# Kernel tuning notes

Measured on AMD Instinct MI355X. Metric: run time of the kernel, lower is better.

Reference implementation:

```python
import jax, jax.numpy as jnp
import numpy as np
from jax import lax

VOCAB, EMBED, HIDDEN, OUT = 256, 256, 512, 256
B, T = 256, 1024


def setup_inputs() -> dict:
    key = jax.random.key(0)
    k1, k2, k3, k4, k5, k6 = jax.random.split(key, 6)
    x = jax.random.randint(k1, (B, T), 0, VOCAB)
    h = jnp.zeros((B, HIDDEN), dtype=jnp.float32)
    emb = jax.random.normal(k2, (VOCAB, EMBED), dtype=jnp.float32)
    # torch Linear weights are [out_features, in_features]
    W = jax.random.normal(k3, (HIDDEN, EMBED + HIDDEN), dtype=jnp.float32) * 0.02
    b = jax.random.normal(k4, (HIDDEN,), dtype=jnp.float32) * 0.02
    Wd = jax.random.normal(k5, (OUT, HIDDEN), dtype=jnp.float32) * 0.02
    bd = jax.random.normal(k6, (OUT,), dtype=jnp.float32) * 0.02
    return {"x": x, "h": h, "emb": emb, "W": W, "b": b, "Wd": Wd, "bd": bd}


def reference(x, h, emb, W, b, Wd, bd):
    # Embed all timesteps at once: [B, T, E] -> time-major [T, B, E]
    ex = jnp.swapaxes(emb[x], 0, 1)

    # Split recurrent weight into input and hidden parts so concat is a sum of GEMMs.
    Wx = W[:, :EMBED]      # [H, E]
    Wh = W[:, EMBED:]      # [H, H]

    def step(h_prev, e_t):
        h_next = jnp.tanh(e_t @ Wx.T + h_prev @ Wh.T + b)
        return h_next, h_next

    h_final, hs = lax.scan(step, h, ex)          # hs: [T, B, H]
    outputs = jnp.swapaxes(hs, 0, 1) @ Wd.T + bd  # [B, T, OUT]
    return outputs, h_final
```

## Files before the change

kernel.cpp:

```cpp
#include <hip/hip_runtime.h>

typedef float f32x4 __attribute__((ext_vector_type(4)));
typedef int i32x4 __attribute__((ext_vector_type(4)));

#define B_ 256
#define T_ 1024
#define H_ 512
#define E_ 256
#define O_ 256
#define V_ 256

__device__ __align__(16) unsigned g_P2[V_ * 256];
__device__ __align__(16) signed char    g_Whq[H_ * H_];
__device__ float                        g_scale[H_];
__device__ __align__(16) signed char    g_Wdq[O_ * H_];
__device__ float                        g_sd[O_];

__device__ __forceinline__ unsigned short f2bf(float f) {
    union { float f; unsigned int u; } v; v.f = f;
    unsigned int r = v.u + 0x7fffu + ((v.u >> 16) & 1u);
    return (unsigned short)(r >> 16);
}
__device__ __forceinline__ float bf2f(unsigned short s) {
    union { unsigned int u; float f; } v; v.u = ((unsigned int)s) << 16;
    return v.f;
}
#define SW16(r_) (((r_) & 15) << 4)

__global__ void k_embWx(const float* __restrict__ emb, const float* __restrict__ W,
                        const float* __restrict__ bb) {
    __shared__ float e[E_];
    int v = blockIdx.x;
    e[threadIdx.x] = emb[(size_t)v * E_ + threadIdx.x];
    __syncthreads();
#pragma unroll
    for (int rep = 0; rep < 2; rep++) {
        int n = threadIdx.x + rep * 256;
        const float4* wr4 = (const float4*)(W + (size_t)n * (E_ + H_));
        float s = bb[n];
        for (int k = 0; k < E_ / 4; k++) {
            float4 wv = wr4[k];
            s += e[4*k] * wv.x + e[4*k+1] * wv.y + e[4*k+2] * wv.z + e[4*k+3] * wv.w;
        }
        int w = n >> 6, r6 = n & 63;
        int lo = r6 & 15, nt = r6 >> 4;
        int p = nt >> 1, half = nt & 1;
        ((unsigned short*)g_P2)[(v * 256 + w * 32 + lo * 2 + p) * 2 + half] = f2bf(s);
    }
}

__global__ void k_prep8(const float* __restrict__ W) {
    const int n = blockIdx.x;
    const int li = threadIdx.x;
    const float* src = W + (size_t)n * (E_ + H_) + E_;
    float v[8];
    float mx = 0.f;
#pragma unroll
    for (int m = 0; m < 8; m++) { v[m] = src[li * 8 + m]; mx = fmaxf(mx, fabsf(v[m])); }
#pragma unroll
    for (int off = 1; off < 64; off <<= 1)
        mx = fmaxf(mx, __shfl_xor(mx, off));
    const float s = fmaxf(mx, 1e-20f) / 127.f;
    if (li == 0) g_scale[n] = s;
    const float inv = 1.f / s;
    unsigned long long pk = 0;
#pragma unroll
    for (int m = 0; m < 8; m++) {
        int q = __float2int_rn(v[m] * inv);
        q = q > 127 ? 127 : (q < -127 ? -127 : q);
        pk |= ((unsigned long long)(unsigned char)(signed char)q) << (8 * m);
    }
    const int ktt = li >> 3;
    const int hig = (li >> 1) & 3;
    const int jh = li & 1;
    *(unsigned long long*)(g_Whq + (((size_t)(n >> 4) * 8 + ktt) * 1024)
                           + ((n & 15) + (hig << 4)) * 16 + jh * 8) = pk;
}

__global__ void k_prepWd8(const float* __restrict__ Wd) {
    const int n = blockIdx.x;
    const int li = threadIdx.x;
    const float* src = Wd + (size_t)n * H_;
    float v[8];
    float mx = 0.f;
#pragma unroll
    for (int m = 0; m < 8; m++) { v[m] = src[li * 8 + m]; mx = fmaxf(mx, fabsf(v[m])); }
#pragma unroll
    for (int off = 1; off < 64; off <<= 1)
        mx = fmaxf(mx, __shfl_xor(mx, off));
    const float s = fmaxf(mx, 1e-20f) / 127.f;
    if (li == 0) g_sd[n] = s;
    const float inv = 1.f / s;
    unsigned long long pk = 0;
#pragma unroll
    for (int m = 0; m < 8; m++) {
        int q = __float2int_rn(v[m] * inv);
        q = q > 127 ? 127 : (q < -127 ? -127 : q);
        pk |= ((unsigned long long)(unsigned char)(signed char)q) << (8 * m);
    }
    const int ktt = li >> 3;
    const int hig = (li >> 1) & 3;
    const int jh = li & 1;
    *(unsigned long long*)(g_Wdq + (((size_t)(n >> 4) * 8 + ktt) * 1024)
                           + ((n & 15) + (hig << 4)) * 16 + jh * 8) = pk;
}

__global__ void __launch_bounds__(512) k_rnn(const int* __restrict__ x,
                                             const float* __restrict__ h0,
                                             float* __restrict__ out) {
    __shared__ __align__(16) signed char lds_img[2][16 * 512];
    __shared__ __align__(16) signed char lds_W[128 * 1024];
    const int tid = threadIdx.x;
    const int w = tid >> 6, l = tid & 63;
    const int hi = l >> 4, lo = l & 15;
    const int r0 = blockIdx.x * 16;
    const int w4 = w * 4;
    const int nb = w * 64 + lo;
    const int swl = SW16(lo);

    i32x4 breg[4][4];
#pragma unroll
    for (int nt = 0; nt < 4; nt++)
#pragma unroll
        for (int kt = 0; kt < 4; kt++)
            breg[nt][kt] = *(const i32x4*)(g_Whq + ((w4 + nt) * 8 + kt) * 1024 + l * 16);

#pragma unroll
    for (int nt = 0; nt < 4; nt++)
#pragma unroll
        for (int kk = 0; kk < 4; kk++) {
            i32x4 v = *(const i32x4*)(g_Whq + ((w4 + nt) * 8 + 4 + kk) * 1024 + l * 16);
            *(i32x4*)(lds_W + ((w4 + nt) * 4 + kk) * 1024 + l * 16) = v;
        }

    float gs[4];
#pragma unroll
    for (int nt = 0; nt < 4; nt++) gs[nt] = g_scale[nb + nt * 16] * (1.f / 127.f);

    {
        const int row = tid >> 5;
        const int c0 = (tid & 31) * 16;
        const float* hp = h0 + (size_t)(r0 + row) * H_ + c0;
        union { unsigned char b[16]; uint4 v; } pk;
#pragma unroll
        for (int i = 0; i < 16; i++) {
            int qq = __float2int_rn(fminf(fmaxf(hp[i], -1.f), 1.f) * 127.f);
            pk.b[i] = (unsigned char)(signed char)qq;
        }
        *(uint4*)(lds_img[0] + row * 512 + (c0 ^ SW16(row))) = pk.v;
    }

    const int xr = r0 + hi * 4;
    int xs0 = x[(xr + 0) * T_], xs1 = x[(xr + 1) * T_],
        xs2 = x[(xr + 2) * T_], xs3 = x[(xr + 3) * T_];

    unsigned char* hsb = (unsigned char*)out;
    float* hfin = out + (size_t)B_ * T_ * O_;
    __syncthreads();

#pragma unroll 1
    for (int t = 0; t < T_; t++) {
        const signed char* img = lds_img[t & 1];

        if (t) {
            const int row = tid >> 5;
            const int cb = (tid & 31) * 16;
            uint4 d = *(const uint4*)(img + row * 512 + (cb ^ SW16(row)));
            *(uint4*)(hsb + (size_t)(r0 + row) * (T_ * 1024) + (size_t)(t - 1) * 1024 + cb) = d;
        }

        unsigned up[4][2];
        {
            const int pb = (w << 5) + (lo << 1);
            *(uint2*)&up[0][0] = *(const uint2*)(g_P2 + (xs0 << 8) + pb);
            *(uint2*)&up[1][0] = *(const uint2*)(g_P2 + (xs1 << 8) + pb);
            *(uint2*)&up[2][0] = *(const uint2*)(g_P2 + (xs2 << 8) + pb);
            *(uint2*)&up[3][0] = *(const uint2*)(g_P2 + (xs3 << 8) + pb);
        }
        {
            const int tn = (t < T_ - 1) ? t + 1 : t;
            xs0 = x[(xr + 0) * T_ + tn]; xs1 = x[(xr + 1) * T_ + tn];
            xs2 = x[(xr + 2) * T_ + tn]; xs3 = x[(xr + 3) * T_ + tn];
        }

        i32x4 acc[4];
#pragma unroll
        for (int nt = 0; nt < 4; nt++) { acc[nt][0] = 0; acc[nt][1] = 0; acc[nt][2] = 0; acc[nt][3] = 0; }
#pragma unroll
        for (int kt = 0; kt < 4; kt++) {
            i32x4 a = *(const i32x4*)(img + lo * 512 + ((kt * 64 + hi * 16) ^ swl));
            acc[0] = __builtin_amdgcn_mfma_i32_16x16x64_i8(a, breg[0][kt], acc[0], 0, 0, 0);
            acc[1] = __builtin_amdgcn_mfma_i32_16x16x64_i8(a, breg[1][kt], acc[1], 0, 0, 0);
            acc[2] = __builtin_amdgcn_mfma_i32_16x16x64_i8(a, breg[2][kt], acc[2], 0, 0, 0);
            acc[3] = __builtin_amdgcn_mfma_i32_16x16x64_i8(a, breg[3][kt], acc[3], 0, 0, 0);
        }
#pragma unroll
        for (int kk = 0; kk < 4; kk++) {
            i32x4 a = *(const i32x4*)(img + lo * 512 + (((4 + kk) * 64 + hi * 16) ^ swl));
            i32x4 b0 = *(const i32x4*)(lds_W + ((w4 + 0) * 4 + kk) * 1024 + l * 16);
            i32x4 b1 = *(const i32x4*)(lds_W + ((w4 + 1) * 4 + kk) * 1024 + l * 16);
            i32x4 b2 = *(const i32x4*)(lds_W + ((w4 + 2) * 4 + kk) * 1024 + l * 16);
            i32x4 b3 = *(const i32x4*)(lds_W + ((w4 + 3) * 4 + kk) * 1024 + l * 16);
            acc[0] = __builtin_amdgcn_mfma_i32_16x16x64_i8(a, b0, acc[0], 0, 0, 0);
            acc[1] = __builtin_amdgcn_mfma_i32_16x16x64_i8(a, b1, acc[1], 0, 0, 0);
            acc[2] = __builtin_amdgcn_mfma_i32_16x16x64_i8(a, b2, acc[2], 0, 0, 0);
            acc[3] = __builtin_amdgcn_mfma_i32_16x16x64_i8(a, b3, acc[3], 0, 0, 0);
        }

        signed char* imw = lds_img[(t & 1) ^ 1];
#pragma unroll
        for (int nt = 0; nt < 4; nt++) {
            const int nn = nb + nt * 16;
#pragma unroll
            for (int rg = 0; rg < 4; rg++) {
                const int r = hi * 4 + rg;
                const unsigned uw = up[rg][nt >> 1];
                const float uf = bf2f((nt & 1) ? (unsigned short)(uw >> 16)
                                               : (unsigned short)(uw & 0xffffu));
                float f = __builtin_fmaf((float)acc[nt][rg], gs[nt], uf);
                float kf = f * 2.885390081777927f;
                float E; asm("v_exp_f32 %0, %1" : "=v"(E) : "v"(kf));
                float d1 = E + 1.f;
                float r1; asm("v_rcp_f32 %0, %1" : "=v"(r1) : "v"(d1));
                float qf = __builtin_fmaf(-254.f, r1, 127.f);
                int q = __float2int_rn(qf);
                imw[r * 512 + (nn ^ SW16(r))] = (signed char)q;
                if (t == T_ - 1) hfin[(r0 + r) * H_ + nn] = qf * (1.f / 127.f);
            }
        }

        __builtin_amdgcn_sched_barrier(0);
        asm volatile("s_waitcnt lgkmcnt(0)" ::: "memory");
        __builtin_amdgcn_s_barrier();
        __builtin_amdgcn_sched_barrier(0);
    }

    {
        const int row = tid >> 5;
        const int cb = (tid & 31) * 16;
        uint4 d = *(const uint4*)(lds_img[0] + row * 512 + (cb ^ SW16(row)));
        *(uint4*)(hsb + (size_t)(r0 + row) * (T_ * 1024) + (size_t)(T_ - 1) * 1024 + cb) = d;
    }
}

__launch_bounds__(512, 2)
__global__ void k_out(const float* __restrict__ bd, float* out) {
    int tid = threadIdx.x;
    int w = tid >> 6, l = tid & 63;
    int hi = l >> 4, lo = l & 15;
    size_t m0 = (size_t)blockIdx.x * 256 + w * 32;
    const unsigned char* hsb = (const unsigned char*)out;
    float bdv[16], sdl[16];
#pragma unroll
    for (int nt = 0; nt < 16; nt++) {
        bdv[nt] = bd[nt * 16 + lo];
        sdl[nt] = g_sd[nt * 16 + lo] * (1.f / 127.f);
    }
    i32x4 acc[2][16];
#pragma unroll
    for (int m = 0; m < 2; m++)
#pragma unroll
        for (int nt = 0; nt < 16; nt++) { acc[m][nt][0] = 0; acc[m][nt][1] = 0; acc[m][nt][2] = 0; acc[m][nt][3] = 0; }
#pragma unroll 2
    for (int kt = 0; kt < 8; kt++) {
        i32x4 a0 = *(const i32x4*)(hsb + (m0 + lo) * 1024 + kt * 64 + hi * 16);
        i32x4 a1 = *(const i32x4*)(hsb + (m0 + 16 + lo) * 1024 + kt * 64 + hi * 16);
#pragma unroll
        for (int nt = 0; nt < 16; nt++) {
            i32x4 bf = *(const i32x4*)(g_Wdq + (nt * 8 + kt) * 1024 + l * 16);
            acc[0][nt] = __builtin_amdgcn_mfma_i32_16x16x64_i8(a0, bf, acc[0][nt], 0, 0, 0);
            acc[1][nt] = __builtin_amdgcn_mfma_i32_16x16x64_i8(a1, bf, acc[1][nt], 0, 0, 0);
        }
    }
#pragma unroll
    for (int m = 0; m < 2; m++)
#pragma unroll
        for (int nt = 0; nt < 16; nt++)
#pragma unroll
            for (int rg = 0; rg < 4; rg++) {
                size_t row = m0 + m * 16 + hi * 4 + rg;
                out[row * O_ + nt * 16 + lo] = (float)acc[m][nt][rg] * sdl[nt] + bdv[nt];
            }
}

extern "C" void kernel_launch(void* const* d_in, const int* in_sizes, int n_in,
                              void* d_out, int out_size, void* d_ws, size_t ws_size,
                              hipStream_t stream) {
    const int*   x   = (const int*)d_in[0];
    const float* h0  = (const float*)d_in[1];
    const float* emb = (const float*)d_in[2];
    const float* W   = (const float*)d_in[3];
    const float* b   = (const float*)d_in[4];
    const float* Wd  = (const float*)d_in[5];
    const float* bd  = (const float*)d_in[6];
    float* out = (float*)d_out;

    k_embWx<<<dim3(V_), dim3(256), 0, stream>>>(emb, W, b);
    k_prep8<<<dim3(H_), dim3(64), 0, stream>>>(W);
    k_prepWd8<<<dim3(O_), dim3(64), 0, stream>>>(Wd);
    k_rnn<<<dim3(16), dim3(512), 0, stream>>>(x, h0, out);
    k_out<<<dim3(1024), dim3(512), 0, stream>>>(bd, out);
}
```

Baseline: 1.820 ms.

## Fold input projection into int accumulator init and use rational tanh approximation

```diff
diff --git a/kernel.cpp b/kernel.cpp
--- a/kernel.cpp
+++ b/kernel.cpp
@@ -10,7 +10,7 @@
 #define O_ 256
 #define V_ 256
 
-__device__ __align__(16) unsigned g_P2[V_ * 256];
+__device__ __align__(16) int g_P3[V_ * H_];
 __device__ __align__(16) signed char    g_Whq[H_ * H_];
 __device__ float                        g_scale[H_];
 __device__ __align__(16) signed char    g_Wdq[O_ * H_];
@@ -21,11 +21,63 @@
     unsigned int r = v.u + 0x7fffu + ((v.u >> 16) & 1u);
     return (unsigned short)(r >> 16);
 }
-__device__ __forceinline__ float bf2f(unsigned short s) {
-    union { unsigned int u; float f; } v; v.u = ((unsigned int)s) << 16;
-    return v.f;
-}
 #define SW16(r_) (((r_) & 15) << 4)
+
+__global__ void k_prep8(const float* __restrict__ W) {
+    const int n = blockIdx.x;
+    const int li = threadIdx.x;
+    const float* src = W + (size_t)n * (E_ + H_) + E_;
+    float v[8];
+    float mx = 0.f;
+#pragma unroll
+    for (int m = 0; m < 8; m++) { v[m] = src[li * 8 + m]; mx = fmaxf(mx, fabsf(v[m])); }
+#pragma unroll
+    for (int off = 1; off < 64; off <<= 1)
+        mx = fmaxf(mx, __shfl_xor(mx, off));
+    const float s = fmaxf(mx, 1e-20f) / 127.f;
+    if (li == 0) g_scale[n] = s;
+    const float inv = 1.f / s;
+    unsigned long long pk = 0;
+#pragma unroll
+    for (int m = 0; m < 8; m++) {
+        int q = __float2int_rn(v[m] * inv);
+        q = q > 127 ? 127 : (q < -127 ? -127 : q);
+        pk |= ((unsigned long long)(unsigned char)(signed char)q) << (8 * m);
+    }
+    const int ktt = li >> 3;
+    const int hig = (li >> 1) & 3;
+    const int jh = li & 1;
+    *(unsigned long long*)(g_Whq + (((size_t)(n >> 4) * 8 + ktt) * 1024)
+                           + ((n & 15) + (hig << 4)) * 16 + jh * 8) = pk;
+}
+
+__global__ void k_prepWd8(const float* __restrict__ Wd) {
+    const int n = blockIdx.x;
+    const int li = threadIdx.x;
+    const float* src = Wd + (size_t)n * H_;
+    float v[8];
+    float mx = 0.f;
+#pragma unroll
+    for (int m = 0; m < 8; m++) { v[m] = src[li * 8 + m]; mx = fmaxf(mx, fabsf(v[m])); }
+#pragma unroll
+    for (int off = 1; off < 64; off <<= 1)
+        mx = fmaxf(mx, __shfl_xor(mx, off));
+    const float s = fmaxf(mx, 1e-20f) / 127.f;
+    if (li == 0) g_sd[n] = s;
+    const float inv = 1.f / s;
+    unsigned long long pk = 0;
+#pragma unroll
+    for (int m = 0; m < 8; m++) {
+        int q = __float2int_rn(v[m] * inv);
+        q = q > 127 ? 127 : (q < -127 ? -127 : q);
+        pk |= ((unsigned long long)(unsigned char)(signed char)q) << (8 * m);
+    }
+    const int ktt = li >> 3;
+    const int hig = (li >> 1) & 3;
+    const int jh = li & 1;
+    *(unsigned long long*)(g_Wdq + (((size_t)(n >> 4) * 8 + ktt) * 1024)
+                           + ((n & 15) + (hig << 4)) * 16 + jh * 8) = pk;
+}
 
 __global__ void k_embWx(const float* __restrict__ emb, const float* __restrict__ W,
                         const float* __restrict__ bb) {
@@ -44,65 +96,9 @@
         }
         int w = n >> 6, r6 = n & 63;
         int lo = r6 & 15, nt = r6 >> 4;
-        int p = nt >> 1, half = nt & 1;
-        ((unsigned short*)g_P2)[(v * 256 + w * 32 + lo * 2 + p) * 2 + half] = f2bf(s);
-    }
-}
-
-__global__ void k_prep8(const float* __restrict__ W) {
-    const int n = blockIdx.x;
-    const int li = threadIdx.x;
-    const float* src = W + (size_t)n * (E_ + H_) + E_;
-    float v[8];
-    float mx = 0.f;
-#pragma unroll
-    for (int m = 0; m < 8; m++) { v[m] = src[li * 8 + m]; mx = fmaxf(mx, fabsf(v[m])); }
-#pragma unroll
-    for (int off = 1; off < 64; off <<= 1)
-        mx = fmaxf(mx, __shfl_xor(mx, off));
-    const float s = fmaxf(mx, 1e-20f) / 127.f;
-    if (li == 0) g_scale[n] = s;
-    const float inv = 1.f / s;
-    unsigned long long pk = 0;
-#pragma unroll
-    for (int m = 0; m < 8; m++) {
-        int q = __float2int_rn(v[m] * inv);
-        q = q > 127 ? 127 : (q < -127 ? -127 : q);
-        pk |= ((unsigned long long)(unsigned char)(signed char)q) << (8 * m);
-    }
-    const int ktt = li >> 3;
-    const int hig = (li >> 1) & 3;
-    const int jh = li & 1;
-    *(unsigned long long*)(g_Whq + (((size_t)(n >> 4) * 8 + ktt) * 1024)
-                           + ((n & 15) + (hig << 4)) * 16 + jh * 8) = pk;
-}
-
-__global__ void k_prepWd8(const float* __restrict__ Wd) {
-    const int n = blockIdx.x;
-    const int li = threadIdx.x;
-    const float* src = Wd + (size_t)n * H_;
-    float v[8];
-    float mx = 0.f;
-#pragma unroll
-    for (int m = 0; m < 8; m++) { v[m] = src[li * 8 + m]; mx = fmaxf(mx, fabsf(v[m])); }
-#pragma unroll
-    for (int off = 1; off < 64; off <<= 1)
-        mx = fmaxf(mx, __shfl_xor(mx, off));
-    const float s = fmaxf(mx, 1e-20f) / 127.f;
-    if (li == 0) g_sd[n] = s;
-    const float inv = 1.f / s;
-    unsigned long long pk = 0;
-#pragma unroll
-    for (int m = 0; m < 8; m++) {
-        int q = __float2int_rn(v[m] * inv);
-        q = q > 127 ? 127 : (q < -127 ? -127 : q);
-        pk |= ((unsigned long long)(unsigned char)(signed char)q) << (8 * m);
-    }
-    const int ktt = li >> 3;
-    const int hig = (li >> 1) & 3;
-    const int jh = li & 1;
-    *(unsigned long long*)(g_Wdq + (((size_t)(n >> 4) * 8 + ktt) * 1024)
-                           + ((n & 15) + (hig << 4)) * 16 + jh * 8) = pk;
+        g_P3[v * 512 + w * 64 + lo * 4 + nt] =
+            __float2int_rn(s * 127.f / g_scale[n]);
+    }
 }
 
 __global__ void __launch_bounds__(512) k_rnn(const int* __restrict__ x,
@@ -151,8 +147,13 @@
     }
 
     const int xr = r0 + hi * 4;
+    const int p3b = (w << 6) + (lo << 2);
     int xs0 = x[(xr + 0) * T_], xs1 = x[(xr + 1) * T_],
         xs2 = x[(xr + 2) * T_], xs3 = x[(xr + 3) * T_];
+    i32x4 u40 = *(const i32x4*)(g_P3 + (xs0 << 9) + p3b);
+    i32x4 u41 = *(const i32x4*)(g_P3 + (xs1 << 9) + p3b);
+    i32x4 u42 = *(const i32x4*)(g_P3 + (xs2 << 9) + p3b);
+    i32x4 u43 = *(const i32x4*)(g_P3 + (xs3 << 9) + p3b);
 
     unsigned char* hsb = (unsigned char*)out;
     float* hfin = out + (size_t)B_ * T_ * O_;
@@ -169,23 +170,22 @@
             *(uint4*)(hsb + (size_t)(r0 + row) * (T_ * 1024) + (size_t)(t - 1) * 1024 + cb) = d;
         }
 
-        unsigned up[4][2];
-        {
-            const int pb = (w << 5) + (lo << 1);
-            *(uint2*)&up[0][0] = *(const uint2*)(g_P2 + (xs0 << 8) + pb);
-            *(uint2*)&up[1][0] = *(const uint2*)(g_P2 + (xs1 << 8) + pb);
-            *(uint2*)&up[2][0] = *(const uint2*)(g_P2 + (xs2 << 8) + pb);
-            *(uint2*)&up[3][0] = *(const uint2*)(g_P2 + (xs3 << 8) + pb);
+        i32x4 acc[4];
+#pragma unroll
+        for (int nt = 0; nt < 4; nt++) {
+            acc[nt][0] = u40[nt]; acc[nt][1] = u41[nt];
+            acc[nt][2] = u42[nt]; acc[nt][3] = u43[nt];
         }
         {
             const int tn = (t < T_ - 1) ? t + 1 : t;
             xs0 = x[(xr + 0) * T_ + tn]; xs1 = x[(xr + 1) * T_ + tn];
             xs2 = x[(xr + 2) * T_ + tn]; xs3 = x[(xr + 3) * T_ + tn];
-        }
-
-        i32x4 acc[4];
-#pragma unroll
-        for (int nt = 0; nt < 4; nt++) { acc[nt][0] = 0; acc[nt][1] = 0; acc[nt][2] = 0; acc[nt][3] = 0; }
+            u40 = *(const i32x4*)(g_P3 + (xs0 << 9) + p3b);
+            u41 = *(const i32x4*)(g_P3 + (xs1 << 9) + p3b);
+            u42 = *(const i32x4*)(g_P3 + (xs2 << 9) + p3b);
+            u43 = *(const i32x4*)(g_P3 + (xs3 << 9) + p3b);
+        }
+
 #pragma unroll
         for (int kt = 0; kt < 4; kt++) {
             i32x4 a = *(const i32x4*)(img + lo * 512 + ((kt * 64 + hi * 16) ^ swl));
@@ -214,18 +214,18 @@
 #pragma unroll
             for (int rg = 0; rg < 4; rg++) {
                 const int r = hi * 4 + rg;
-                const unsigned uw = up[rg][nt >> 1];
-                const float uf = bf2f((nt & 1) ? (unsigned short)(uw >> 16)
-                                               : (unsigned short)(uw & 0xffffu));
-                float f = __builtin_fmaf((float)acc[nt][rg], gs[nt], uf);
-                float kf = f * 2.885390081777927f;
-                float E; asm("v_exp_f32 %0, %1" : "=v"(E) : "v"(kf));
-                float d1 = E + 1.f;
-                float r1; asm("v_rcp_f32 %0, %1" : "=v"(r1) : "v"(d1));
-                float qf = __builtin_fmaf(-254.f, r1, 127.f);
-                int q = __float2int_rn(qf);
+                float f = (float)acc[nt][rg] * gs[nt];
+                f = fminf(fmaxf(f, -4.f), 4.f);
+                float uu = f * f;
+                float np = __builtin_fmaf(uu, uu + 105.f, 945.f);
+                float num = f * np;
+                float dp = __builtin_fmaf(uu, 15.f, 420.f);
+                float den = __builtin_fmaf(uu, dp, 945.f);
+                float r1; asm("v_rcp_f32 %0, %1" : "=v"(r1) : "v"(den));
+                float th = num * r1;
+                int q = __float2int_rn(th * 127.f);
                 imw[r * 512 + (nn ^ SW16(r))] = (signed char)q;
-                if (t == T_ - 1) hfin[(r0 + r) * H_ + nn] = qf * (1.f / 127.f);
+                if (t == T_ - 1) hfin[(r0 + r) * H_ + nn] = th;
             }
         }
 
@@ -295,9 +295,9 @@
     const float* bd  = (const float*)d_in[6];
     float* out = (float*)d_out;
 
-    k_embWx<<<dim3(V_), dim3(256), 0, stream>>>(emb, W, b);
     k_prep8<<<dim3(H_), dim3(64), 0, stream>>>(W);
     k_prepWd8<<<dim3(O_), dim3(64), 0, stream>>>(Wd);
+    k_embWx<<<dim3(V_), dim3(256), 0, stream>>>(emb, W, b);
     k_rnn<<<dim3(16), dim3(512), 0, stream>>>(x, h0, out);
     k_out<<<dim3(1024), dim3(512), 0, stream>>>(bd, out);
 }
```

Result: slower. 1.977 ms (+8.6%).
